# Kernel tuning notes

Hardware: AMD Instinct MI355X
Metric: run time of the kernel (lower is better)

The kernel has to match this reference:

```python
import jax, jax.numpy as jnp
import numpy as np
import math

B, S, D, H, HD, W, G = 2, 4096, 768, 12, 64, 256, 64  # batch, seq, embed, heads, head_dim, one-sided window, n global tokens


def _chunk_keys(k, w):
    # k: [B,S,H,HD] -> overlapping 3w-wide key windows per w-sized query chunk: [B,nc,3w,H,HD]
    Bz, S_, Hh, HDd = k.shape
    nc = S_ // w
    kp = jnp.pad(k, ((0, 0), (w, w), (0, 0), (0, 0)))
    kb = kp.reshape(Bz, nc + 2, w, Hh, HDd)
    return jnp.concatenate([kb[:, 0:nc], kb[:, 1:nc + 1], kb[:, 2:nc + 2]], axis=2)


def _band_qk(q, k, w):
    # banded scores: out[b,i,h,j] = q_i . k_{i+j-w}, j in [0, 2w]
    Bz, S_, Hh, HDd = q.shape
    nc = S_ // w
    qc = q.reshape(Bz, nc, w, Hh, HDd)
    kc = _chunk_keys(k, w)
    sc = jnp.einsum('bcphd,bckhd->bchpk', qc, kc)  # [B,nc,H,w,3w]
    rows = jnp.arange(w)[:, None]
    cols = rows + jnp.arange(2 * w + 1)[None, :]   # within-window key index = p + j
    band = sc[:, :, :, rows, cols]                 # [B,nc,H,w,2w+1]
    return band.transpose(0, 1, 3, 2, 4).reshape(Bz, S_, Hh, 2 * w + 1)


def _band_pv(p, v, w):
    # out[b,i,h,:] = sum_j p[b,i,h,j] * v[b, i+j-w, h, :]
    Bz, S_, Hh, K = p.shape
    HDd = v.shape[-1]
    nc = S_ // w
    pc = p.reshape(Bz, nc, w, Hh, K).transpose(0, 1, 3, 2, 4)  # [B,nc,H,w,2w+1]
    rows = jnp.arange(w)[:, None]
    cols = rows + jnp.arange(2 * w + 1)[None, :]
    full = jnp.zeros((Bz, nc, Hh, w, 3 * w), p.dtype).at[:, :, :, rows, cols].set(pc)
    vc = _chunk_keys(v, w)
    out = jnp.einsum('bchpk,bckhd->bcphd', full, vc)  # [B,nc,w,H,HD]
    return out.reshape(Bz, S_, Hh, HDd)


def setup_inputs() -> dict:
    key = jax.random.key(0)
    ks = jax.random.split(key, 4)
    std = 0.02
    # attention mask: +1 = global (first G tokens), 0 = local windowed, no padding
    attention_mask = jnp.concatenate(
        [jnp.ones((B, G), jnp.int32), jnp.zeros((B, S - G), jnp.int32)], axis=1)
    return {
        'hidden_states': jax.random.normal(ks[0], (B, S, D), jnp.float32),
        'attention_mask': attention_mask,
        'Wq': jax.random.normal(ks[1], (D, D), jnp.float32) * std,
        'bq': jnp.zeros((D,), jnp.float32),
        'Wk': jax.random.normal(ks[2], (D, D), jnp.float32) * std,
        'bk': jnp.zeros((D,), jnp.float32),
        'Wv': jax.random.normal(ks[3], (D, D), jnp.float32) * std,
        'bv': jnp.zeros((D,), jnp.float32),
    }


def reference(hidden_states, attention_mask, Wq, bq, Wk, bk, Wv, bv):
    Bz, S_, D_ = hidden_states.shape
    HDd = D_ // H
    q = ((hidden_states @ Wq.T + bq) / math.sqrt(HDd)).reshape(Bz, S_, H, HDd)
    k = (hidden_states @ Wk.T + bk).reshape(Bz, S_, H, HDd)
    v = (hidden_states @ Wv.T + bv).reshape(Bz, S_, H, HDd)

    band = _band_qk(q, k, W)  # [B,S,H,2W+1]

    i = jnp.arange(S_)
    key_abs = i[:, None] + jnp.arange(2 * W + 1)[None, :] - W  # [S,2W+1]
    valid = (key_abs >= 0) & (key_abs < S_)
    kac = jnp.clip(key_abs, 0, S_ - 1)
    is_glob = attention_mask != 0                       # [B,S]
    glob_at_key = is_glob[:, kac] & valid[None]          # [B,S,2W+1]
    # remove global keys from windowed attention: d_mask = -10000 * head_dim (ones @ float_mask)
    band = band + jnp.where(glob_at_key, jnp.float32(-10000.0 * HDd), jnp.float32(0.0))[:, :, None, :]
    # mask_invalid_locations: out-of-range diagonals -> -inf
    band = jnp.where(valid[None, :, None, :], band, -jnp.inf)

    # global-token attention (first G tokens are the global ones)
    gs = jnp.einsum('bihd,bghd->bihg', q, k[:, :G])      # [B,S,H,G]

    scores = jnp.concatenate([gs, band], axis=-1)        # [B,S,H,G+2W+1]
    probs = jax.nn.softmax(scores.astype(jnp.float32), axis=-1)

    attn = jnp.einsum('bihg,bghd->bihd', probs[..., :G], v[:, :G]) + _band_pv(probs[..., G:], v, W)
    # [B,S,H,HD] -> (seq_len, bsz, embed_dim) as in the torch module
    return jnp.transpose(attn, (1, 0, 2, 3)).reshape(S_, Bz, D_)
```

## Files before the change

kernel.cpp:

```cpp
#include <hip/hip_runtime.h>
#include <hip/hip_bf16.h>
#include <stdint.h>

typedef __attribute__((ext_vector_type(4))) float          f32x4;
typedef __attribute__((ext_vector_type(4))) float          f4;
typedef __attribute__((ext_vector_type(2))) unsigned int   u32x2;
typedef __bf16 bf16_t;
typedef __attribute__((ext_vector_type(8))) bf16_t         bf16x8;
typedef __attribute__((ext_vector_type(8))) unsigned short u16x8;
typedef __attribute__((ext_vector_type(4))) unsigned short u16x4;

#define NB 2
#define NS 4096
#define ND 768
#define NH 12
#define NW 256

__device__ __forceinline__ unsigned short f2bf(float f) {
  union { float f; unsigned u; } v; v.f = f;
  unsigned r = v.u + 0x7fffu + ((v.u >> 16) & 1u);
  return (unsigned short)(r >> 16);
}

__device__ __forceinline__ unsigned pack2bf(float a, float b) {
  return (unsigned)f2bf(a) | ((unsigned)f2bf(b) << 16);
}

__device__ __forceinline__ float exp2_fast(float x) {
  float r;
  asm("v_exp_f32 %0, %1" : "=v"(r) : "v"(x));
  return r;
}

__device__ __forceinline__ void gload16(const void* g, void* l) {
  __builtin_amdgcn_global_load_lds((const __attribute__((address_space(1))) void*)g,
                                   (__attribute__((address_space(3))) void*)l, 16, 0, 0);
}

__global__ void cast_kernel(const float* __restrict__ in, unsigned short* __restrict__ out, int n4) {
  int i = blockIdx.x * blockDim.x + threadIdx.x;
  int stride = gridDim.x * blockDim.x;
  for (; i < n4; i += stride) {
    f4 v = reinterpret_cast<const f4*>(in)[i];
    u32x2 o = {pack2bf(v.x, v.y), pack2bf(v.z, v.w)};
    reinterpret_cast<u32x2*>(out)[i] = o;
  }
}

__global__ void cast3_kernel(const float* __restrict__ w0, const float* __restrict__ w1,
                             const float* __restrict__ w2, unsigned short* __restrict__ o0,
                             unsigned short* __restrict__ o1, unsigned short* __restrict__ o2) {
  const int n4 = 768 * 768 / 4;
  int i = blockIdx.x * blockDim.x + threadIdx.x;
  int stride = gridDim.x * blockDim.x;
  for (; i < 3 * n4; i += stride) {
    int m = i / n4, j = i - m * n4;
    const float* in = (m == 0) ? w0 : ((m == 1) ? w1 : w2);
    unsigned short* out = (m == 0) ? o0 : ((m == 1) ? o1 : o2);
    f4 v = reinterpret_cast<const f4*>(in)[j];
    u32x2 o = {pack2bf(v.x, v.y), pack2bf(v.z, v.w)};
    reinterpret_cast<u32x2*>(out)[j] = o;
  }
}

__global__ __launch_bounds__(256) void qkv_gemm(
    const unsigned short* __restrict__ Ab,
    const unsigned short* __restrict__ Wqb,
    const unsigned short* __restrict__ Wkb,
    const unsigned short* __restrict__ Wvb,
    const float* __restrict__ bqp, const float* __restrict__ bkp, const float* __restrict__ bvp,
    unsigned short* __restrict__ Qw, unsigned short* __restrict__ Kw, unsigned short* __restrict__ Vw) {
  __shared__ unsigned short smem[2][2][128 * 32];

  int phys = blockIdx.x;
  int logical = (phys & 7) * 144 + (phys >> 3);
  int bn = logical % 18, bm = logical / 18;
  int mat = bn / 6, bnn = bn % 6;
  const unsigned short* Wm = (mat == 0) ? Wqb : ((mat == 1) ? Wkb : Wvb);
  const float* bias = (mat == 0) ? bqp : ((mat == 1) ? bkp : bvp);
  unsigned short* dst = (mat == 0) ? Qw : ((mat == 1) ? Kw : Vw);

  int t = threadIdx.x;
  int w = t >> 6, l = t & 63;
  int lg = l >> 4, ln = l & 15;
  int wm = w & 1, wn = w >> 1;

  f32x4 acc[4][4];
#pragma unroll
  for (int i = 0; i < 4; i++)
#pragma unroll
    for (int j = 0; j < 4; j++) acc[i][j] = f32x4{0.f, 0.f, 0.f, 0.f};

#pragma unroll
  for (int is = 0; is < 2; ++is) {
    int chunk = is * 256 + t;
    int row = chunk >> 2;
    int c8 = (chunk & 3) * 8;
    gload16(Ab + ((size_t)(bm * 128 + row)) * 768 + c8, &smem[0][0][chunk * 8]);
    gload16(Wm + ((size_t)(bnn * 128 + row)) * 768 + c8, &smem[0][1][chunk * 8]);
  }
  __syncthreads();

  for (int kt = 0; kt < 24; ++kt) {
    int cur = kt & 1;
    if (kt < 23) {
#pragma unroll
      for (int is = 0; is < 2; ++is) {
        int chunk = is * 256 + t;
        int row = chunk >> 2;
        int c8 = (chunk & 3) * 8;
        gload16(Ab + ((size_t)(bm * 128 + row)) * 768 + (kt + 1) * 32 + c8,
                &smem[cur ^ 1][0][chunk * 8]);
        gload16(Wm + ((size_t)(bnn * 128 + row)) * 768 + (kt + 1) * 32 + c8,
                &smem[cur ^ 1][1][chunk * 8]);
      }
    }
    bf16x8 af[4], bfr[4];
#pragma unroll
    for (int i = 0; i < 4; i++) {
      af[i]  = *reinterpret_cast<const bf16x8*>(&smem[cur][0][(wm * 64 + i * 16 + ln) * 32 + lg * 8]);
      bfr[i] = *reinterpret_cast<const bf16x8*>(&smem[cur][1][(wn * 64 + i * 16 + ln) * 32 + lg * 8]);
    }
#pragma unroll
    for (int i = 0; i < 4; i++)
#pragma unroll
      for (int j = 0; j < 4; j++)
        acc[i][j] = __builtin_amdgcn_mfma_f32_16x16x32_bf16(af[i], bfr[j], acc[i][j], 0, 0, 0);
    __syncthreads();
  }

  unsigned short* ep = &smem[0][0][0];
#pragma unroll
  for (int j = 0; j < 4; j++) {
    int col = wn * 64 + j * 16 + ln;
    float bv_ = bias[bnn * 128 + col];
#pragma unroll
    for (int i = 0; i < 4; i++) {
#pragma unroll
      for (int r = 0; r < 4; r++) {
        int row = wm * 64 + i * 16 + lg * 4 + r;
        float v = acc[i][j][r] + bv_;
        if (mat == 0) v *= 0.1803368801111244f;
        int g = col >> 3;
        ep[row * 128 + (((g ^ (row & 15)) << 3) | (col & 7))] = f2bf(v);
      }
    }
  }
  __syncthreads();
  {
    int row = t >> 1, half = t & 1;
    int tok = bm * 128 + row;
    int bb = tok >> 12, ss = tok & 4095;
    int head = bnn * 2 + half;
    unsigned short* drow = dst + (((size_t)bb * 12 + head) * 4096 + ss) * 64;
#pragma unroll
    for (int kk8 = 0; kk8 < 8; ++kk8) {
      int g = (half * 8 + kk8) ^ (row & 15);
      *reinterpret_cast<u16x8*>(drow + kk8 * 8) =
          *reinterpret_cast<const u16x8*>(ep + row * 128 + g * 8);
    }
  }
}

__global__ __launch_bounds__(512) void attn_kernel(
    const unsigned short* __restrict__ Qw,
    const unsigned short* __restrict__ Kw,
    const unsigned short* __restrict__ Vw,
    const int* __restrict__ amask,
    float* __restrict__ out) {
  __shared__ unsigned short Ks[2][64 * 64];
  __shared__ unsigned short Vt[2][64 * 64];
  __shared__ unsigned Msk[128];

  int phys = blockIdx.x;
  int logical = (phys & 7) * 96 + (phys >> 3);
  int qc = logical & 31;
  int bh = logical >> 5;
  int b = bh / 12;
  int hh = bh % 12;
  int qbase = qc * 128;

  int t = threadIdx.x, w = t >> 6, l = t & 63;
  int lg = l >> 4, ln = l & 15;

  const unsigned short* Qbh = Qw + (size_t)bh * (NS * 64);
  const unsigned short* Kbh = Kw + (size_t)bh * (NS * 64);
  const unsigned short* Vbh = Vw + (size_t)bh * (NS * 64);
  const int* mrow = amask + b * NS;

#pragma unroll
  for (int r8 = 0; r8 < 8; ++r8) {
    int wp = r8 * 8 + w;
    unsigned long long bal = __ballot(mrow[wp * 64 + l] != 0);
    if (l == 0) {
      Msk[wp * 2] = (unsigned)bal;
      Msk[wp * 2 + 1] = (unsigned)(bal >> 32);
    }
  }

  int q = qbase + w * 16 + ln;
  int qwmin = qbase + w * 16;

  bf16x8 qf[2];
  {
    const unsigned short* qp = Qbh + (size_t)q * 64 + lg * 8;
    qf[0] = *reinterpret_cast<const bf16x8*>(qp);
    qf[1] = *reinterpret_cast<const bf16x8*>(qp + 32);
  }

  float m_s = -1e30f, l_s = 0.f;
  f32x4 oacc[4];
#pragma unroll
  for (int i = 0; i < 4; i++) oacc[i] = f32x4{0.f, 0.f, 0.f, 0.f};

  int tt_lo = (qbase >= 256) ? 0 : ((256 - qbase) >> 6);
  int tt_hi_raw = (NS + 192 - qbase) >> 6;
  int tt_hi = tt_hi_raw < 9 ? tt_hi_raw : 9;
  int ntl = tt_hi - tt_lo + 2;

  int krow = t >> 3, gran = t & 7;
  int p2 = t & 31, d0v = (t >> 5) * 4;

  {
    gload16(Kbh + (size_t)krow * 64 + (gran ^ (krow & 7)) * 8, &Ks[0][0] + t * 8);
    const unsigned short* vp0 = Vbh + (size_t)(2 * p2) * 64 + d0v;
    u16x4 va = *reinterpret_cast<const u16x4*>(vp0);
    u16x4 vb = *reinterpret_cast<const u16x4*>(vp0 + 64);
#pragma unroll
    for (int j = 0; j < 4; ++j) {
      int d = d0v + j;
      unsigned val = (unsigned)va[j] | ((unsigned)vb[j] << 16);
      *reinterpret_cast<unsigned*>(&Vt[0][0] + d * 64 + ((2 * p2) ^ ((d & 15) << 2))) = val;
    }
  }
  __syncthreads();

  for (int idx = 0; idx < ntl; ++idx) {
    int cur = idx & 1;
    int key0 = (idx == 0) ? 0 : (qbase - 256 + (tt_lo + idx - 1) * 64);
    bool has_next = (idx + 1) < ntl;

    u16x4 va, vb;
    if (has_next) {
      int nk0 = qbase - 256 + (tt_lo + idx) * 64;
      gload16(Kbh + (size_t)(nk0 + krow) * 64 + (gran ^ (krow & 7)) * 8,
              &Ks[cur ^ 1][0] + t * 8);
      const unsigned short* vp0 = Vbh + (size_t)(nk0 + 2 * p2) * 64 + d0v;
      va = *reinterpret_cast<const u16x4*>(vp0);
      vb = *reinterpret_cast<const u16x4*>(vp0 + 64);
    }

    bool relevant = (idx == 0) ||
                    ((key0 + 63 >= qwmin - 256) && (key0 <= qwmin + 15 + 256));
    if (relevant) {
      const unsigned short* ksb = &Ks[cur][0];
      f32x4 sa[4];
#pragma unroll
      for (int nt = 0; nt < 4; nt++) sa[nt] = f32x4{0.f, 0.f, 0.f, 0.f};
#pragma unroll
      for (int nt = 0; nt < 4; nt++) {
        int key = nt * 16 + ln;
#pragma unroll
        for (int ks = 0; ks < 2; ++ks) {
          int dby = (ks * 64 + lg * 16) ^ ((key & 7) << 4);
          bf16x8 kf = *reinterpret_cast<const bf16x8*>(ksb + key * 64 + (dby >> 1));
          sa[nt] = __builtin_amdgcn_mfma_f32_16x16x32_bf16(kf, qf[ks], sa[nt], 0, 0, 0);
        }
      }

      if (idx > 0) {
        unsigned mw0 = Msk[key0 >> 5], mw1 = Msk[(key0 >> 5) + 1];
        bool clean = ((mw0 | mw1) == 0) && (key0 >= qwmin - 241) && (key0 <= qwmin + 193);
        if (!clean) {
#pragma unroll
          for (int nt = 0; nt < 4; nt++) {
            unsigned mword = (nt & 2) ? mw1 : mw0;
#pragma unroll
            for (int r = 0; r < 4; r++) {
              int key = key0 + 16 * nt + 4 * lg + r;
              bool sup = (mword >> ((16 * (nt & 1) + 4 * lg + r) & 31)) & 1;
              bool bad = sup || ((unsigned)(key - q + NW) > 2u * NW);
              if (bad) sa[nt][r] = -1e30f;
            }
          }
        }
      }

      float tmax = sa[0][0];
#pragma unroll
      for (int nt = 0; nt < 4; nt++)
#pragma unroll
        for (int r = 0; r < 4; r++) tmax = fmaxf(tmax, sa[nt][r]);
      if (!__all(tmax - m_s <= 8.f)) {
        tmax = fmaxf(tmax, __shfl_xor(tmax, 16, 64));
        tmax = fmaxf(tmax, __shfl_xor(tmax, 32, 64));
        float mn = fmaxf(m_s, tmax);
        float scl = exp2_fast(m_s - mn);
        m_s = mn;
        l_s *= scl;
#pragma unroll
        for (int i = 0; i < 4; i++) oacc[i] *= scl;
      }
#pragma unroll
      for (int nt = 0; nt < 4; nt++)
#pragma unroll
        for (int r = 0; r < 4; r++) {
          float p = exp2_fast(sa[nt][r] - m_s);
          sa[nt][r] = p;
          l_s += p;
        }

      union { bf16_t bb[8]; bf16x8 v; } pf0, pf1;
#pragma unroll
      for (int r = 0; r < 4; r++) {
        pf0.bb[r]     = (bf16_t)sa[0][r];
        pf0.bb[4 + r] = (bf16_t)sa[1][r];
        pf1.bb[r]     = (bf16_t)sa[2][r];
        pf1.bb[4 + r] = (bf16_t)sa[3][r];
      }

      const unsigned short* vtb = &Vt[cur][0];
#pragma unroll
      for (int ks = 0; ks < 2; ++ks) {
        bf16x8 pv = ks ? pf1.v : pf0.v;
#pragma unroll
        for (int nt = 0; nt < 4; ++nt) {
          int d = nt * 16 + ln;
          int sw = (d & 15) << 2;
          int e0 = (32 * ks + 4 * lg) ^ sw;
          int e1 = (32 * ks + 16 + 4 * lg) ^ sw;
          union { u16x4 h[2]; bf16x8 v; } vf;
          vf.h[0] = *reinterpret_cast<const u16x4*>(vtb + d * 64 + e0);
          vf.h[1] = *reinterpret_cast<const u16x4*>(vtb + d * 64 + e1);
          oacc[nt] = __builtin_amdgcn_mfma_f32_16x16x32_bf16(vf.v, pv, oacc[nt], 0, 0, 0);
        }
      }
    }

    if (has_next) {
      unsigned short* vtn = &Vt[cur ^ 1][0];
#pragma unroll
      for (int j = 0; j < 4; ++j) {
        int d = d0v + j;
        unsigned val = (unsigned)va[j] | ((unsigned)vb[j] << 16);
        *reinterpret_cast<unsigned*>(vtn + d * 64 + ((2 * p2) ^ ((d & 15) << 2))) = val;
      }
    }
    __syncthreads();
  }

  l_s += __shfl_xor(l_s, 16, 64);
  l_s += __shfl_xor(l_s, 32, 64);
  float inv = 1.0f / l_s;
  float* orow = out + ((size_t)q * NB + b) * ND + hh * 64;
#pragma unroll
  for (int nt = 0; nt < 4; nt++) {
    f4 o;
#pragma unroll
    for (int r = 0; r < 4; r++) o[r] = oacc[nt][r] * inv;
    *reinterpret_cast<f4*>(orow + nt * 16 + 4 * lg) = o;
  }
}

extern "C" void kernel_launch(void* const* d_in, const int* in_sizes, int n_in,
                              void* d_out, int out_size, void* d_ws, size_t ws_size,
                              hipStream_t stream) {
  (void)in_sizes; (void)n_in; (void)out_size; (void)ws_size;
  const float* hidden = (const float*)d_in[0];
  const int*   amask  = (const int*)d_in[1];
  const float* Wq = (const float*)d_in[2];
  const float* bq = (const float*)d_in[3];
  const float* Wk = (const float*)d_in[4];
  const float* bk = (const float*)d_in[5];
  const float* Wv = (const float*)d_in[6];
  const float* bv = (const float*)d_in[7];
  float* out = (float*)d_out;

  char* p = (char*)d_ws;
  unsigned short* hb  = (unsigned short*)p; p += (size_t)8192 * 768 * 2;
  unsigned short* wqb = (unsigned short*)p; p += (size_t)768 * 768 * 2;
  unsigned short* wkb = (unsigned short*)p; p += (size_t)768 * 768 * 2;
  unsigned short* wvb = (unsigned short*)p; p += (size_t)768 * 768 * 2;
  unsigned short* Qws = (unsigned short*)p; p += (size_t)24 * 4096 * 64 * 2;
  unsigned short* Kws = (unsigned short*)p; p += (size_t)24 * 4096 * 64 * 2;
  unsigned short* Vws = (unsigned short*)p; p += (size_t)24 * 4096 * 64 * 2;

  cast_kernel<<<1024, 256, 0, stream>>>(hidden, hb, 8192 * 768 / 4);
  cast3_kernel<<<432, 256, 0, stream>>>(Wq, Wk, Wv, wqb, wkb, wvb);
  qkv_gemm<<<64 * 18, 256, 0, stream>>>(hb, wqb, wkb, wvb, bq, bk, bv, Qws, Kws, Vws);
  attn_kernel<<<24 * 32, 512, 0, stream>>>(Qws, Kws, Vws, amask, out);
}
```

Before: 193.0 us.

## Triple-buffer QKV GEMM loads with vmcnt waits and merge cast kernels

The QKV projection GEMM moves from double to triple-buffered LDS staging. It prefetches two k-tiles ahead and swaps the full __syncthreads for a partial s_waitcnt vmcnt plus a raw barrier, so global-to-LDS loads overlap more MFMA work. The two fp32-to-bf16 cast kernels are merged into one launch to remove a kernel boundary. LDS use grows by half, which may reduce occupancy, and the hand-written vmcnt counts must match the number of outstanding loads.

```diff
diff --git a/kernel.cpp b/kernel.cpp
--- a/kernel.cpp
+++ b/kernel.cpp
@@ -37,26 +37,26 @@
                                    (__attribute__((address_space(3))) void*)l, 16, 0, 0);
 }
 
-__global__ void cast_kernel(const float* __restrict__ in, unsigned short* __restrict__ out, int n4) {
+__global__ void cast_all(const float* __restrict__ hidden,
+                         const float* __restrict__ w0, const float* __restrict__ w1,
+                         const float* __restrict__ w2,
+                         unsigned short* __restrict__ hb,
+                         unsigned short* __restrict__ o0, unsigned short* __restrict__ o1,
+                         unsigned short* __restrict__ o2) {
+  const int nh4 = 8192 * 768 / 4;
+  const int nw4 = 768 * 768 / 4;
+  const int total = nh4 + 3 * nw4;
   int i = blockIdx.x * blockDim.x + threadIdx.x;
   int stride = gridDim.x * blockDim.x;
-  for (; i < n4; i += stride) {
-    f4 v = reinterpret_cast<const f4*>(in)[i];
-    u32x2 o = {pack2bf(v.x, v.y), pack2bf(v.z, v.w)};
-    reinterpret_cast<u32x2*>(out)[i] = o;
-  }
-}
-
-__global__ void cast3_kernel(const float* __restrict__ w0, const float* __restrict__ w1,
-                             const float* __restrict__ w2, unsigned short* __restrict__ o0,
-                             unsigned short* __restrict__ o1, unsigned short* __restrict__ o2) {
-  const int n4 = 768 * 768 / 4;
-  int i = blockIdx.x * blockDim.x + threadIdx.x;
-  int stride = gridDim.x * blockDim.x;
-  for (; i < 3 * n4; i += stride) {
-    int m = i / n4, j = i - m * n4;
-    const float* in = (m == 0) ? w0 : ((m == 1) ? w1 : w2);
-    unsigned short* out = (m == 0) ? o0 : ((m == 1) ? o1 : o2);
+  for (; i < total; i += stride) {
+    const float* in; unsigned short* out; int j;
+    if (i < nh4) { in = hidden; out = hb; j = i; }
+    else {
+      int k = i - nh4, m = k / nw4;
+      j = k - m * nw4;
+      in = (m == 0) ? w0 : ((m == 1) ? w1 : w2);
+      out = (m == 0) ? o0 : ((m == 1) ? o1 : o2);
+    }
     f4 v = reinterpret_cast<const f4*>(in)[j];
     u32x2 o = {pack2bf(v.x, v.y), pack2bf(v.z, v.w)};
     reinterpret_cast<u32x2*>(out)[j] = o;
@@ -70,7 +70,7 @@
     const unsigned short* __restrict__ Wvb,
     const float* __restrict__ bqp, const float* __restrict__ bkp, const float* __restrict__ bvp,
     unsigned short* __restrict__ Qw, unsigned short* __restrict__ Kw, unsigned short* __restrict__ Vw) {
-  __shared__ unsigned short smem[2][2][128 * 32];
+  __shared__ unsigned short smem[3][2][128 * 32];
 
   int phys = blockIdx.x;
   int logical = (phys & 7) * 144 + (phys >> 3);
@@ -85,50 +85,59 @@
   int lg = l >> 4, ln = l & 15;
   int wm = w & 1, wn = w >> 1;
 
+  int srow = t >> 2;
+  int sc8 = (t & 3) * 8;
+
   f32x4 acc[4][4];
 #pragma unroll
   for (int i = 0; i < 4; i++)
 #pragma unroll
     for (int j = 0; j < 4; j++) acc[i][j] = f32x4{0.f, 0.f, 0.f, 0.f};
 
-#pragma unroll
-  for (int is = 0; is < 2; ++is) {
-    int chunk = is * 256 + t;
-    int row = chunk >> 2;
-    int c8 = (chunk & 3) * 8;
-    gload16(Ab + ((size_t)(bm * 128 + row)) * 768 + c8, &smem[0][0][chunk * 8]);
-    gload16(Wm + ((size_t)(bnn * 128 + row)) * 768 + c8, &smem[0][1][chunk * 8]);
-  }
-  __syncthreads();
-
+  auto stage = [&](int kt, int buf) {
+#pragma unroll
+    for (int is = 0; is < 2; ++is) {
+      int chunk = is * 256 + t;
+      int row = (is << 6) + srow;
+      gload16(Ab + ((size_t)(bm * 128 + row)) * 768 + kt * 32 + sc8, &smem[buf][0][chunk * 8]);
+      gload16(Wm + ((size_t)(bnn * 128 + row)) * 768 + kt * 32 + sc8, &smem[buf][1][chunk * 8]);
+    }
+  };
+
+  stage(0, 0);
+  stage(1, 1);
+  asm volatile("s_waitcnt vmcnt(4)" ::: "memory");
+  __builtin_amdgcn_s_barrier();
+  __builtin_amdgcn_sched_barrier(0);
+
+  int buf = 0;
   for (int kt = 0; kt < 24; ++kt) {
-    int cur = kt & 1;
-    if (kt < 23) {
-#pragma unroll
-      for (int is = 0; is < 2; ++is) {
-        int chunk = is * 256 + t;
-        int row = chunk >> 2;
-        int c8 = (chunk & 3) * 8;
-        gload16(Ab + ((size_t)(bm * 128 + row)) * 768 + (kt + 1) * 32 + c8,
-                &smem[cur ^ 1][0][chunk * 8]);
-        gload16(Wm + ((size_t)(bnn * 128 + row)) * 768 + (kt + 1) * 32 + c8,
-                &smem[cur ^ 1][1][chunk * 8]);
-      }
+    if (kt < 22) {
+      int nb = buf + 2; nb = (nb >= 3) ? nb - 3 : nb;
+      stage(kt + 2, nb);
     }
     bf16x8 af[4], bfr[4];
 #pragma unroll
     for (int i = 0; i < 4; i++) {
-      af[i]  = *reinterpret_cast<const bf16x8*>(&smem[cur][0][(wm * 64 + i * 16 + ln) * 32 + lg * 8]);
-      bfr[i] = *reinterpret_cast<const bf16x8*>(&smem[cur][1][(wn * 64 + i * 16 + ln) * 32 + lg * 8]);
+      af[i]  = *reinterpret_cast<const bf16x8*>(&smem[buf][0][(wm * 64 + i * 16 + ln) * 32 + lg * 8]);
+      bfr[i] = *reinterpret_cast<const bf16x8*>(&smem[buf][1][(wn * 64 + i * 16 + ln) * 32 + lg * 8]);
     }
 #pragma unroll
     for (int i = 0; i < 4; i++)
 #pragma unroll
       for (int j = 0; j < 4; j++)
         acc[i][j] = __builtin_amdgcn_mfma_f32_16x16x32_bf16(af[i], bfr[j], acc[i][j], 0, 0, 0);
-    __syncthreads();
-  }
-
+
+    if (kt < 23) {
+      if (kt < 22) asm volatile("s_waitcnt vmcnt(4)" ::: "memory");
+      else         asm volatile("s_waitcnt vmcnt(0)" ::: "memory");
+      __builtin_amdgcn_s_barrier();
+      __builtin_amdgcn_sched_barrier(0);
+    }
+    buf = (buf == 2) ? 0 : buf + 1;
+  }
+
+  __syncthreads();
   unsigned short* ep = &smem[0][0][0];
 #pragma unroll
   for (int j = 0; j < 4; j++) {
@@ -385,8 +394,7 @@
   unsigned short* Kws = (unsigned short*)p; p += (size_t)24 * 4096 * 64 * 2;
   unsigned short* Vws = (unsigned short*)p; p += (size_t)24 * 4096 * 64 * 2;
 
-  cast_kernel<<<1024, 256, 0, stream>>>(hidden, hb, 8192 * 768 / 4);
-  cast3_kernel<<<432, 256, 0, stream>>>(Wq, Wk, Wv, wqb, wkb, wvb);
+  cast_all<<<2048, 256, 0, stream>>>(hidden, Wq, Wk, Wv, hb, wqb, wkb, wvb);
   qkv_gemm<<<64 * 18, 256, 0, stream>>>(hb, wqb, wkb, wvb, bq, bk, bv, Qws, Kws, Vws);
   attn_kernel<<<24 * 32, 512, 0, stream>>>(Qws, Kws, Vws, amask, out);
 }
```

After: 188.8 us. 1.02x faster.
